# Kernel tuning notes

Hardware: AMD Instinct MI355X
Metric: run time of the kernel (lower is better)

Reference implementation:

```python
import jax, jax.numpy as jnp
import numpy as np

NUM_HEADS = 16


def setup_inputs() -> dict:
    key = jax.random.key(0)
    ks = jax.random.split(key, 6)
    B, S, D = 2, 2048, 1024
    hidden_states = jax.random.normal(ks[0], (B, S, D), dtype=jnp.float32)
    attention_mask = jnp.zeros((B, 1, 1, S), dtype=jnp.float32)  # additive mask
    # Linear weights stored as [in, out] (equivalent to torch weight.T)
    W_qkv = jax.random.normal(ks[1], (D, 3 * D), dtype=jnp.float32) * (1.0 / np.sqrt(D))
    b_qkv = jnp.zeros((3 * D,), dtype=jnp.float32)
    W_proj = jax.random.normal(ks[2], (D, D), dtype=jnp.float32) * (1.0 / np.sqrt(D))
    b_proj = jnp.zeros((D,), dtype=jnp.float32)
    return {
        "hidden_states": hidden_states,
        "attention_mask": attention_mask,
        "W_qkv": W_qkv,
        "b_qkv": b_qkv,
        "W_proj": W_proj,
        "b_proj": b_proj,
    }


def reference(hidden_states, attention_mask, W_qkv, b_qkv, W_proj, b_proj):
    B, S, D = hidden_states.shape
    H = NUM_HEADS
    hd = D // H
    scale = 1.0 / jnp.sqrt(jnp.asarray(hd, hidden_states.dtype))

    qkv = hidden_states @ W_qkv + b_qkv            # [B,S,3D]
    q, k, v = jnp.split(qkv, 3, axis=-1)
    # [B,S,D] -> [B,H,S,hd]
    split_heads = lambda t: t.reshape(B, S, H, hd).transpose(0, 2, 1, 3)
    q, k, v = split_heads(q), split_heads(k), split_heads(v)

    scores = jnp.einsum("bhqd,bhkd->bhqk", q, k) * scale + attention_mask
    attn = jax.nn.softmax(scores, axis=-1)
    ctx = jnp.einsum("bhqk,bhkd->bhqd", attn, v)   # [B,H,S,hd]
    ctx = ctx.transpose(0, 2, 1, 3).reshape(B, S, D)
    return ctx @ W_proj + b_proj
```

## Files before the change

kernel.cpp:

```cpp
#include <hip/hip_runtime.h>
#include <hip/hip_bf16.h>

typedef short short8 __attribute__((ext_vector_type(8)));
typedef float floatx4 __attribute__((ext_vector_type(4)));
typedef int intx4 __attribute__((ext_vector_type(4)));
typedef int intx2 __attribute__((ext_vector_type(2)));

#define S_LEN 2048
#define DMODEL 1024
#define NH 16
#define HD 64
#define BATCH 2

static __device__ __forceinline__ short f2bf(float x) {
    __hip_bfloat16 h = __float2bfloat16(x);
    return *(short*)&h;
}

static __device__ __forceinline__ unsigned pk2(float lo, float hi) {
    unsigned a = (unsigned)(unsigned short)f2bf(lo);
    unsigned b = (unsigned)(unsigned short)f2bf(hi);
    return a | (b << 16);
}

static __device__ __forceinline__ void async_ld16(const __hip_bfloat16* g, __hip_bfloat16* l) {
    __builtin_amdgcn_global_load_lds(
        (const __attribute__((address_space(1))) unsigned int*)g,
        (__attribute__((address_space(3))) unsigned int*)l, 16, 0, 0);
}

__global__ __launch_bounds__(256) void cvt_kernel(const float* __restrict__ X,
                                                  __hip_bfloat16* __restrict__ Y) {
    int i = (blockIdx.x * 256 + threadIdx.x) * 8;
    floatx4 f0 = *(const floatx4*)&X[i];
    floatx4 f1 = *(const floatx4*)&X[i + 4];
    short8 s;
    s[0] = f2bf(f0[0]); s[1] = f2bf(f0[1]); s[2] = f2bf(f0[2]); s[3] = f2bf(f0[3]);
    s[4] = f2bf(f1[0]); s[5] = f2bf(f1[1]); s[6] = f2bf(f1[2]); s[7] = f2bf(f1[3]);
    *(short8*)&Y[i] = s;
}

__global__ void transpose_kernel(const float* __restrict__ W,
                                 __hip_bfloat16* __restrict__ Wt, int K, int N) {
    __shared__ float tile[32][33];
    int n0 = blockIdx.x * 32, k0 = blockIdx.y * 32;
    int tx = threadIdx.x, ty = threadIdx.y;
#pragma unroll
    for (int i = 0; i < 32; i += 8)
        tile[ty + i][tx] = W[(size_t)(k0 + ty + i) * N + n0 + tx];
    __syncthreads();
#pragma unroll
    for (int i = 0; i < 32; i += 8)
        Wt[(size_t)(n0 + ty + i) * K + k0 + tx] = __float2bfloat16(tile[tx][ty + i]);
}

__global__ __launch_bounds__(256) void gemm128(
    const __hip_bfloat16* __restrict__ A, const __hip_bfloat16* __restrict__ Bt,
    const float* __restrict__ bias, float* __restrict__ Cf,
    __hip_bfloat16* __restrict__ Qp, __hip_bfloat16* __restrict__ Kp,
    __hip_bfloat16* __restrict__ Vt, int M, int N, int K, int mode) {
    __shared__ __align__(16) __hip_bfloat16 As[2][128 * 32];
    __shared__ __align__(16) __hip_bfloat16 Bs[2][128 * 32];
    const int gx = gridDim.x, gy = gridDim.y;
    const int flat = blockIdx.y * gx + blockIdx.x;
    const int cpx = (gx * gy) >> 3;
    const int id2 = (flat & 7) * cpx + (flat >> 3);
    const int m0 = (id2 % gy) * 128, n0 = (id2 / gy) * 128;
    const int t = threadIdx.x;
    const int wave = t >> 6, lane = t & 63;
    const int quad = lane >> 4, m16 = lane & 15;
    const int wm = (wave >> 1) * 64, wn = (wave & 1) * 64;
    const int srow = lane >> 2, scol = (lane & 3) * 8;

    const int rb0 = wave * 32, rb1 = wave * 32 + 16;
    const size_t aoff0 = (size_t)(m0 + rb0 + srow) * K + scol;
    const size_t aoff1 = (size_t)(m0 + rb1 + srow) * K + scol;
    const size_t boff0 = (size_t)(n0 + rb0 + srow) * K + scol;
    const size_t boff1 = (size_t)(n0 + rb1 + srow) * K + scol;

    async_ld16(&A[aoff0], &As[0][rb0 * 32]);
    async_ld16(&A[aoff1], &As[0][rb1 * 32]);
    async_ld16(&Bt[boff0], &Bs[0][rb0 * 32]);
    async_ld16(&Bt[boff1], &Bs[0][rb1 * 32]);
    __syncthreads();

    floatx4 acc[4][4] = {};
    const int NI = K >> 5;
    for (int it = 0; it < NI; ++it) {
        const int cur = it & 1;
        if (it < NI - 1) {
            const int k0 = (it + 1) * 32;
            async_ld16(&A[aoff0 + k0], &As[cur ^ 1][rb0 * 32]);
            async_ld16(&A[aoff1 + k0], &As[cur ^ 1][rb1 * 32]);
            async_ld16(&Bt[boff0 + k0], &Bs[cur ^ 1][rb0 * 32]);
            async_ld16(&Bt[boff1 + k0], &Bs[cur ^ 1][rb1 * 32]);
        }
        short8 af[4], bfr[4];
#pragma unroll
        for (int i = 0; i < 4; i++)
            af[i] = *(const short8*)&As[cur][(wm + i * 16 + m16) * 32 + quad * 8];
#pragma unroll
        for (int j = 0; j < 4; j++)
            bfr[j] = *(const short8*)&Bs[cur][(wn + j * 16 + m16) * 32 + quad * 8];
#pragma unroll
        for (int i = 0; i < 4; i++)
#pragma unroll
            for (int j = 0; j < 4; j++)
                acc[i][j] = __builtin_amdgcn_mfma_f32_16x16x32_bf16(af[i], bfr[j], acc[i][j], 0, 0, 0);
        __syncthreads();
    }
    if (mode == 0) {
#pragma unroll
        for (int i = 0; i < 4; i++)
#pragma unroll
            for (int j = 0; j < 4; j++) {
                int col = n0 + wn + j * 16 + m16;
                float bv = bias[col];
#pragma unroll
                for (int r = 0; r < 4; r++) {
                    int row = m0 + wm + i * 16 + quad * 4 + r;
                    Cf[(size_t)row * N + col] = acc[i][j][r] + bv;
                }
            }
    } else if (n0 < 2 * DMODEL) {
#pragma unroll
        for (int i = 0; i < 4; i++)
#pragma unroll
            for (int j = 0; j < 4; j++) {
                int col = n0 + wn + j * 16 + m16;
                float bv = bias[col];
#pragma unroll
                for (int r = 0; r < 4; r++) {
                    int row = m0 + wm + i * 16 + quad * 4 + r;
                    __hip_bfloat16 hv = __float2bfloat16(acc[i][j][r] + bv);
                    int tt = col >> 10, rem = col & 1023;
                    int h = rem >> 6, d = rem & 63;
                    int b = row >> 11, s = row & 2047;
                    if (tt == 0) Qp[((size_t)(b * NH + h) * S_LEN + s) * HD + d] = hv;
                    else         Kp[((size_t)(b * NH + h) * S_LEN + s) * HD + d] = hv;
                }
            }
    } else {
        char* T = (char*)As;
        const int bq = m0 >> 11;
        const int s_base = m0 & 2047;
        for (int p = 0; p < 4; p++) {
            if (wave == p) {
#pragma unroll
                for (int j = 0; j < 4; j++) {
                    const int drow = j * 16 + m16;
                    const float bv = bias[n0 + wn + j * 16 + m16];
                    const int within = (quad & 1) * 4;
#pragma unroll
                    for (int i = 0; i < 4; i++) {
                        const int colc = i * 2 + (quad >> 1);
                        const int physc = colc ^ (drow & 7);
                        intx2 v;
                        v[0] = (int)pk2(acc[i][j][0] + bv, acc[i][j][1] + bv);
                        v[1] = (int)pk2(acc[i][j][2] + bv, acc[i][j][3] + bv);
                        *(intx2*)(T + drow * 128 + physc * 16 + within * 2) = v;
                    }
                }
            }
            __syncthreads();
            {
                const int dl = t >> 2;
                const int sseg = (t & 3) * 16;
                const int c0 = (sseg >> 3) ^ (dl & 7);
                const int c1 = ((sseg >> 3) + 1) ^ (dl & 7);
                short8 a0 = *(const short8*)(T + dl * 128 + c0 * 16);
                short8 a1 = *(const short8*)(T + dl * 128 + c1 * 16);
                const int hh = (n0 - 2 * DMODEL + (p & 1) * 64) >> 6;
                const int sg = s_base + (p >> 1) * 64 + sseg;
                __hip_bfloat16* dst = &Vt[((size_t)(bq * NH + hh) * HD + dl) * S_LEN + sg];
                *(short8*)dst = a0;
                *(short8*)(dst + 8) = a1;
            }
            __syncthreads();
        }
    }
}

__global__ __launch_bounds__(512, 8) void attn_kernel(
    const __hip_bfloat16* __restrict__ Q,
    const __hip_bfloat16* __restrict__ K,
    const __hip_bfloat16* __restrict__ Vt,
    const float* __restrict__ mask,
    __hip_bfloat16* __restrict__ ctx) {
    __shared__ __align__(16) __hip_bfloat16 smem[16384];
    __shared__ float wsm[S_LEN];
    const int bh = blockIdx.x;
    const int b = bh >> 4, h = bh & 15;
    const int t = threadIdx.x, wave = t >> 6, lane = t & 63;
    const int team = wave >> 2, tw = wave & 3;
    const int quad = lane >> 4, m16 = lane & 15;
    const int qbase = blockIdx.y * 64 + tw * 16;
    const int ko = team * (S_LEN / 2);
    const __hip_bfloat16* Qh = Q + (size_t)bh * S_LEN * HD;
    const __hip_bfloat16* Kh = K + (size_t)bh * S_LEN * HD;
    const __hip_bfloat16* Vh = Vt + (size_t)bh * HD * S_LEN;
    const float* mb = mask + (size_t)b * S_LEN;
    const float LOG2E = 1.44269504f;
    const float scale2 = 0.125f * LOG2E;
    const float M_FIX2 = 20.0f * LOG2E;

    __hip_bfloat16* Ksb = smem + team * 8192;
    __hip_bfloat16* Vsb = smem + team * 8192 + 4096;

    {
        floatx4 mv = *(const floatx4*)&mb[t * 4];
        floatx4 wv;
#pragma unroll
        for (int r = 0; r < 4; r++) wv[r] = __builtin_fmaf(mv[r], LOG2E, -M_FIX2);
        *(floatx4*)&wsm[t * 4] = wv;
    }

    const int kr = lane >> 3, kc = lane & 7;
    const int kgoff = (tw * 8 + kr) * HD + ((kc ^ kr) * 8);
    const int vr = lane >> 2, vc = lane & 3;
    const int vd = tw * 16 + vr;
    const int vgoff = vd * S_LEN + (((vc ^ ((vd >> 1) & 3))) * 8);
    __hip_bfloat16* kdst0 = Ksb + tw * 512;
    __hip_bfloat16* kdst1 = Ksb + 2048 + tw * 512;
    __hip_bfloat16* vdst0 = Vsb + tw * 512;
    __hip_bfloat16* vdst1 = Vsb + 2048 + tw * 512;

    short8 aq0 = *(const short8*)&Qh[(size_t)(qbase + m16) * HD + quad * 8];
    short8 aq1 = *(const short8*)&Qh[(size_t)(qbase + m16) * HD + 32 + quad * 8];

    const short ONEB = (short)0x3F80;
    const short8 ones = {ONEB, ONEB, ONEB, ONEB, ONEB, ONEB, ONEB, ONEB};

    async_ld16(&Kh[(size_t)ko * HD + kgoff], kdst0);
    async_ld16(&Vh[(size_t)ko + vgoff], vdst0);
    __syncthreads();

    floatx4 o[4] = {};
    floatx4 lacc = {};
    const int swk = m16 & 7;
    const int e = quad & 1;
    const int C = ((quad & 1) << 1) | (quad >> 1);
    const int vsl = (C ^ ((m16 >> 1) & 3)) * 8;

    const int NIT = (S_LEN / 2) / 32;
    for (int it = 0; it < NIT; it++) {
        const int k0 = it * 32;
        const int cur = it & 1;
        if (it < NIT - 1) {
            async_ld16(&Kh[(size_t)(ko + k0 + 32) * HD + kgoff], cur ? kdst0 : kdst1);
            async_ld16(&Vh[(size_t)(ko + k0 + 32) + vgoff], cur ? vdst0 : vdst1);
        }

        const __hip_bfloat16* Kc = Ksb + cur * 2048;
        floatx4 sc[2] = {};
        __builtin_amdgcn_s_setprio(1);
#pragma unroll
        for (int kt = 0; kt < 2; kt++) {
            const int row = kt * 16 + m16;
            short8 ak0 = *(const short8*)&Kc[row * 64 + ((quad ^ swk) * 8)];
            short8 ak1 = *(const short8*)&Kc[row * 64 + (((quad + 4) ^ swk) * 8)];
            sc[kt] = __builtin_amdgcn_mfma_f32_16x16x32_bf16(ak0, aq0, sc[kt], 0, 0, 0);
            sc[kt] = __builtin_amdgcn_mfma_f32_16x16x32_bf16(ak1, aq1, sc[kt], 0, 0, 0);
        }
        __builtin_amdgcn_s_setprio(0);

        unsigned dk[2][2];
#pragma unroll
        for (int kt = 0; kt < 2; kt++) {
            floatx4 wv = *(const floatx4*)&wsm[ko + k0 + kt * 16 + quad * 4];
            float p0 = __builtin_amdgcn_exp2f(__builtin_fmaf(sc[kt][0], scale2, wv[0]));
            float p1 = __builtin_amdgcn_exp2f(__builtin_fmaf(sc[kt][1], scale2, wv[1]));
            float p2 = __builtin_amdgcn_exp2f(__builtin_fmaf(sc[kt][2], scale2, wv[2]));
            float p3 = __builtin_amdgcn_exp2f(__builtin_fmaf(sc[kt][3], scale2, wv[3]));
            dk[kt][0] = pk2(p0, p1);
            dk[kt][1] = pk2(p2, p3);
        }

        unsigned s0 = e ? dk[0][0] : dk[1][0];
        unsigned s1 = e ? dk[0][1] : dk[1][1];
        unsigned r0 = (unsigned)__builtin_amdgcn_ds_swizzle((int)s0, 0x401F);
        unsigned r1 = (unsigned)__builtin_amdgcn_ds_swizzle((int)s1, 0x401F);
        intx4 wa;
        wa[0] = (int)(e ? r0 : dk[0][0]);
        wa[1] = (int)(e ? r1 : dk[0][1]);
        wa[2] = (int)(e ? dk[1][0] : r0);
        wa[3] = (int)(e ? dk[1][1] : r1);
        short8 ap = *(short8*)&wa;

        const __hip_bfloat16* Vc = Vsb + cur * 2048;
        __builtin_amdgcn_s_setprio(1);
        lacc = __builtin_amdgcn_mfma_f32_16x16x32_bf16(ap, ones, lacc, 0, 0, 0);
#pragma unroll
        for (int tt = 0; tt < 4; tt++) {
            const int d = tt * 16 + m16;
            short8 bv = *(const short8*)&Vc[d * 32 + vsl];
            o[tt] = __builtin_amdgcn_mfma_f32_16x16x32_bf16(ap, bv, o[tt], 0, 0, 0);
        }
        __builtin_amdgcn_s_setprio(0);
        __syncthreads();
    }

    float* xch = (float*)smem;
    const int xi = (tw * 64 + lane) * 21;
    if (team == 1) {
#pragma unroll
        for (int tt = 0; tt < 4; tt++)
#pragma unroll
            for (int r = 0; r < 4; r++) xch[xi + tt * 4 + r] = o[tt][r];
#pragma unroll
        for (int r = 0; r < 4; r++) xch[xi + 16 + r] = lacc[r];
    }
    __syncthreads();
    if (team == 0) {
        float li[4];
#pragma unroll
        for (int r = 0; r < 4; r++) li[r] = 1.0f / (lacc[r] + xch[xi + 16 + r]);
#pragma unroll
        for (int tt = 0; tt < 4; tt++)
#pragma unroll
            for (int r = 0; r < 4; r++) {
                int srow = qbase + quad * 4 + r;
                int d = tt * 16 + m16;
                float v = (o[tt][r] + xch[xi + tt * 4 + r]) * li[r];
                ctx[((size_t)b * S_LEN + srow) * DMODEL + h * HD + d] = __float2bfloat16(v);
            }
    }
}

extern "C" void kernel_launch(void* const* d_in, const int* in_sizes, int n_in,
                              void* d_out, int out_size, void* d_ws, size_t ws_size,
                              hipStream_t stream) {
    (void)in_sizes; (void)n_in; (void)out_size; (void)ws_size;
    const float* hidden = (const float*)d_in[0];
    const float* mask   = (const float*)d_in[1];
    const float* Wqkv   = (const float*)d_in[2];
    const float* bqkv   = (const float*)d_in[3];
    const float* Wproj  = (const float*)d_in[4];
    const float* bproj  = (const float*)d_in[5];
    float* out = (float*)d_out;

    __hip_bfloat16* ws = (__hip_bfloat16*)d_ws;
    const size_t Q4 = 4u * 1024 * 1024;
    __hip_bfloat16* Qp      = ws;
    __hip_bfloat16* Kp      = ws + 1 * Q4;
    __hip_bfloat16* Vt      = ws + 2 * Q4;
    __hip_bfloat16* hid_bf  = ws + 3 * Q4;
    __hip_bfloat16* ctx     = ws + 3 * Q4;
    __hip_bfloat16* Wqkv_t  = ws + 4 * Q4;
    __hip_bfloat16* Wproj_t = ws + 4 * Q4;

    cvt_kernel<<<dim3(4 * 1024 * 1024 / 2048), 256, 0, stream>>>(hidden, hid_bf);
    transpose_kernel<<<dim3(3072 / 32, 1024 / 32), dim3(32, 8), 0, stream>>>(Wqkv, Wqkv_t, 1024, 3072);

    gemm128<<<dim3(3072 / 128, 4096 / 128), 256, 0, stream>>>(
        hid_bf, Wqkv_t, bqkv, nullptr, Qp, Kp, Vt, BATCH * S_LEN, 3 * DMODEL, DMODEL, 1);

    transpose_kernel<<<dim3(1024 / 32, 1024 / 32), dim3(32, 8), 0, stream>>>(Wproj, Wproj_t, 1024, 1024);

    attn_kernel<<<dim3(BATCH * NH, S_LEN / 64), 512, 0, stream>>>(Qp, Kp, Vt, mask, ctx);

    gemm128<<<dim3(1024 / 128, 4096 / 128), 256, 0, stream>>>(
        ctx, Wproj_t, bproj, out, nullptr, nullptr, nullptr, BATCH * S_LEN, DMODEL, DMODEL, 0);
}
```

Measured before the change: 215.2 us.

## Halve attention block to 4 waves, each computing two 16-row query tiles

The attention kernel now runs 256 threads (two teams of two waves) instead of 512, and each wave processes 32 query rows as two 16-row groups. Each K and V fragment read from shared memory is reused for two MFMA groups, and each thread issues twice as many async loads per tile. This cuts LDS reads per MFMA and the per-block wave count. The cost is more accumulator registers per wave and fewer waves to hide latency.

```diff
diff --git a/kernel.cpp b/kernel.cpp
--- a/kernel.cpp
+++ b/kernel.cpp
@@ -181,7 +181,7 @@
     }
 }
 
-__global__ __launch_bounds__(512, 8) void attn_kernel(
+__global__ __launch_bounds__(256, 4) void attn_kernel(
     const __hip_bfloat16* __restrict__ Q,
     const __hip_bfloat16* __restrict__ K,
     const __hip_bfloat16* __restrict__ Vt,
@@ -192,9 +192,9 @@
     const int bh = blockIdx.x;
     const int b = bh >> 4, h = bh & 15;
     const int t = threadIdx.x, wave = t >> 6, lane = t & 63;
-    const int team = wave >> 2, tw = wave & 3;
+    const int team = wave >> 1, tw = wave & 1;
     const int quad = lane >> 4, m16 = lane & 15;
-    const int qbase = blockIdx.y * 64 + tw * 16;
+    const int qbase = blockIdx.y * 64 + tw * 32;
     const int ko = team * (S_LEN / 2);
     const __hip_bfloat16* Qh = Q + (size_t)bh * S_LEN * HD;
     const __hip_bfloat16* Kh = K + (size_t)bh * S_LEN * HD;
@@ -207,36 +207,43 @@
     __hip_bfloat16* Ksb = smem + team * 8192;
     __hip_bfloat16* Vsb = smem + team * 8192 + 4096;
 
-    {
-        floatx4 mv = *(const floatx4*)&mb[t * 4];
+#pragma unroll
+    for (int i = 0; i < 2; i++) {
+        const int idx = (t + i * 256) * 4;
+        floatx4 mv = *(const floatx4*)&mb[idx];
         floatx4 wv;
 #pragma unroll
         for (int r = 0; r < 4; r++) wv[r] = __builtin_fmaf(mv[r], LOG2E, -M_FIX2);
-        *(floatx4*)&wsm[t * 4] = wv;
+        *(floatx4*)&wsm[idx] = wv;
     }
 
     const int kr = lane >> 3, kc = lane & 7;
-    const int kgoff = (tw * 8 + kr) * HD + ((kc ^ kr) * 8);
+    const int kgA = (tw * 16 + kr) * HD + ((kc ^ kr) * 8);
+    const int kgB = (tw * 16 + 8 + kr) * HD + ((kc ^ kr) * 8);
     const int vr = lane >> 2, vc = lane & 3;
-    const int vd = tw * 16 + vr;
-    const int vgoff = vd * S_LEN + (((vc ^ ((vd >> 1) & 3))) * 8);
-    __hip_bfloat16* kdst0 = Ksb + tw * 512;
-    __hip_bfloat16* kdst1 = Ksb + 2048 + tw * 512;
-    __hip_bfloat16* vdst0 = Vsb + tw * 512;
-    __hip_bfloat16* vdst1 = Vsb + 2048 + tw * 512;
-
-    short8 aq0 = *(const short8*)&Qh[(size_t)(qbase + m16) * HD + quad * 8];
-    short8 aq1 = *(const short8*)&Qh[(size_t)(qbase + m16) * HD + 32 + quad * 8];
+    const int vsw = (vc ^ ((vr >> 1) & 3)) * 8;
+    const int vgA = (tw * 32 + vr) * S_LEN + vsw;
+    const int vgB = (tw * 32 + 16 + vr) * S_LEN + vsw;
+    const int kd = tw * 1024, vd = tw * 1024;
+
+    short8 aq[2][2];
+#pragma unroll
+    for (int g = 0; g < 2; g++) {
+        aq[g][0] = *(const short8*)&Qh[(size_t)(qbase + g * 16 + m16) * HD + quad * 8];
+        aq[g][1] = *(const short8*)&Qh[(size_t)(qbase + g * 16 + m16) * HD + 32 + quad * 8];
+    }
 
     const short ONEB = (short)0x3F80;
     const short8 ones = {ONEB, ONEB, ONEB, ONEB, ONEB, ONEB, ONEB, ONEB};
 
-    async_ld16(&Kh[(size_t)ko * HD + kgoff], kdst0);
-    async_ld16(&Vh[(size_t)ko + vgoff], vdst0);
+    async_ld16(&Kh[(size_t)ko * HD + kgA], Ksb + kd);
+    async_ld16(&Kh[(size_t)ko * HD + kgB], Ksb + kd + 512);
+    async_ld16(&Vh[(size_t)ko + vgA], Vsb + vd);
+    async_ld16(&Vh[(size_t)ko + vgB], Vsb + vd + 512);
     __syncthreads();
 
-    floatx4 o[4] = {};
-    floatx4 lacc = {};
+    floatx4 o[2][4] = {};
+    floatx4 lacc[2] = {};
     const int swk = m16 & 7;
     const int e = quad & 1;
     const int C = ((quad & 1) << 1) | (quad >> 1);
@@ -247,83 +254,105 @@
         const int k0 = it * 32;
         const int cur = it & 1;
         if (it < NIT - 1) {
-            async_ld16(&Kh[(size_t)(ko + k0 + 32) * HD + kgoff], cur ? kdst0 : kdst1);
-            async_ld16(&Vh[(size_t)(ko + k0 + 32) + vgoff], cur ? vdst0 : vdst1);
+            const int nb = (cur ^ 1) * 2048;
+            async_ld16(&Kh[(size_t)(ko + k0 + 32) * HD + kgA], Ksb + nb + kd);
+            async_ld16(&Kh[(size_t)(ko + k0 + 32) * HD + kgB], Ksb + nb + kd + 512);
+            async_ld16(&Vh[(size_t)(ko + k0 + 32) + vgA], Vsb + nb + vd);
+            async_ld16(&Vh[(size_t)(ko + k0 + 32) + vgB], Vsb + nb + vd + 512);
         }
 
         const __hip_bfloat16* Kc = Ksb + cur * 2048;
-        floatx4 sc[2] = {};
+        floatx4 sc[2][2] = {};
         __builtin_amdgcn_s_setprio(1);
 #pragma unroll
         for (int kt = 0; kt < 2; kt++) {
             const int row = kt * 16 + m16;
             short8 ak0 = *(const short8*)&Kc[row * 64 + ((quad ^ swk) * 8)];
             short8 ak1 = *(const short8*)&Kc[row * 64 + (((quad + 4) ^ swk) * 8)];
-            sc[kt] = __builtin_amdgcn_mfma_f32_16x16x32_bf16(ak0, aq0, sc[kt], 0, 0, 0);
-            sc[kt] = __builtin_amdgcn_mfma_f32_16x16x32_bf16(ak1, aq1, sc[kt], 0, 0, 0);
+#pragma unroll
+            for (int g = 0; g < 2; g++) {
+                sc[g][kt] = __builtin_amdgcn_mfma_f32_16x16x32_bf16(ak0, aq[g][0], sc[g][kt], 0, 0, 0);
+                sc[g][kt] = __builtin_amdgcn_mfma_f32_16x16x32_bf16(ak1, aq[g][1], sc[g][kt], 0, 0, 0);
+            }
         }
         __builtin_amdgcn_s_setprio(0);
 
-        unsigned dk[2][2];
+        unsigned dk[2][2][2];
 #pragma unroll
         for (int kt = 0; kt < 2; kt++) {
             floatx4 wv = *(const floatx4*)&wsm[ko + k0 + kt * 16 + quad * 4];
-            float p0 = __builtin_amdgcn_exp2f(__builtin_fmaf(sc[kt][0], scale2, wv[0]));
-            float p1 = __builtin_amdgcn_exp2f(__builtin_fmaf(sc[kt][1], scale2, wv[1]));
-            float p2 = __builtin_amdgcn_exp2f(__builtin_fmaf(sc[kt][2], scale2, wv[2]));
-            float p3 = __builtin_amdgcn_exp2f(__builtin_fmaf(sc[kt][3], scale2, wv[3]));
-            dk[kt][0] = pk2(p0, p1);
-            dk[kt][1] = pk2(p2, p3);
-        }
-
-        unsigned s0 = e ? dk[0][0] : dk[1][0];
-        unsigned s1 = e ? dk[0][1] : dk[1][1];
-        unsigned r0 = (unsigned)__builtin_amdgcn_ds_swizzle((int)s0, 0x401F);
-        unsigned r1 = (unsigned)__builtin_amdgcn_ds_swizzle((int)s1, 0x401F);
-        intx4 wa;
-        wa[0] = (int)(e ? r0 : dk[0][0]);
-        wa[1] = (int)(e ? r1 : dk[0][1]);
-        wa[2] = (int)(e ? dk[1][0] : r0);
-        wa[3] = (int)(e ? dk[1][1] : r1);
-        short8 ap = *(short8*)&wa;
+#pragma unroll
+            for (int g = 0; g < 2; g++) {
+                float p0 = __builtin_amdgcn_exp2f(__builtin_fmaf(sc[g][kt][0], scale2, wv[0]));
+                float p1 = __builtin_amdgcn_exp2f(__builtin_fmaf(sc[g][kt][1], scale2, wv[1]));
+                float p2 = __builtin_amdgcn_exp2f(__builtin_fmaf(sc[g][kt][2], scale2, wv[2]));
+                float p3 = __builtin_amdgcn_exp2f(__builtin_fmaf(sc[g][kt][3], scale2, wv[3]));
+                dk[g][kt][0] = pk2(p0, p1);
+                dk[g][kt][1] = pk2(p2, p3);
+            }
+        }
+
+        short8 ap[2];
+#pragma unroll
+        for (int g = 0; g < 2; g++) {
+            unsigned s0 = e ? dk[g][0][0] : dk[g][1][0];
+            unsigned s1 = e ? dk[g][0][1] : dk[g][1][1];
+            unsigned r0 = (unsigned)__builtin_amdgcn_ds_swizzle((int)s0, 0x401F);
+            unsigned r1 = (unsigned)__builtin_amdgcn_ds_swizzle((int)s1, 0x401F);
+            intx4 wa;
+            wa[0] = (int)(e ? r0 : dk[g][0][0]);
+            wa[1] = (int)(e ? r1 : dk[g][0][1]);
+            wa[2] = (int)(e ? dk[g][1][0] : r0);
+            wa[3] = (int)(e ? dk[g][1][1] : r1);
+            ap[g] = *(short8*)&wa;
+        }
 
         const __hip_bfloat16* Vc = Vsb + cur * 2048;
         __builtin_amdgcn_s_setprio(1);
-        lacc = __builtin_amdgcn_mfma_f32_16x16x32_bf16(ap, ones, lacc, 0, 0, 0);
+        lacc[0] = __builtin_amdgcn_mfma_f32_16x16x32_bf16(ap[0], ones, lacc[0], 0, 0, 0);
+        lacc[1] = __builtin_amdgcn_mfma_f32_16x16x32_bf16(ap[1], ones, lacc[1], 0, 0, 0);
 #pragma unroll
         for (int tt = 0; tt < 4; tt++) {
             const int d = tt * 16 + m16;
             short8 bv = *(const short8*)&Vc[d * 32 + vsl];
-            o[tt] = __builtin_amdgcn_mfma_f32_16x16x32_bf16(ap, bv, o[tt], 0, 0, 0);
+            o[0][tt] = __builtin_amdgcn_mfma_f32_16x16x32_bf16(ap[0], bv, o[0][tt], 0, 0, 0);
+            o[1][tt] = __builtin_amdgcn_mfma_f32_16x16x32_bf16(ap[1], bv, o[1][tt], 0, 0, 0);
         }
         __builtin_amdgcn_s_setprio(0);
         __syncthreads();
     }
 
     float* xch = (float*)smem;
-    const int xi = (tw * 64 + lane) * 21;
     if (team == 1) {
 #pragma unroll
-        for (int tt = 0; tt < 4; tt++)
-#pragma unroll
-            for (int r = 0; r < 4; r++) xch[xi + tt * 4 + r] = o[tt][r];
-#pragma unroll
-        for (int r = 0; r < 4; r++) xch[xi + 16 + r] = lacc[r];
+        for (int g = 0; g < 2; g++) {
+            const int xi = ((tw * 2 + g) * 64 + lane) * 21;
+#pragma unroll
+            for (int tt = 0; tt < 4; tt++)
+#pragma unroll
+                for (int r = 0; r < 4; r++) xch[xi + tt * 4 + r] = o[g][tt][r];
+#pragma unroll
+            for (int r = 0; r < 4; r++) xch[xi + 16 + r] = lacc[g][r];
+        }
     }
     __syncthreads();
     if (team == 0) {
-        float li[4];
-#pragma unroll
-        for (int r = 0; r < 4; r++) li[r] = 1.0f / (lacc[r] + xch[xi + 16 + r]);
-#pragma unroll
-        for (int tt = 0; tt < 4; tt++)
-#pragma unroll
-            for (int r = 0; r < 4; r++) {
-                int srow = qbase + quad * 4 + r;
-                int d = tt * 16 + m16;
-                float v = (o[tt][r] + xch[xi + tt * 4 + r]) * li[r];
-                ctx[((size_t)b * S_LEN + srow) * DMODEL + h * HD + d] = __float2bfloat16(v);
-            }
+#pragma unroll
+        for (int g = 0; g < 2; g++) {
+            const int xi = ((tw * 2 + g) * 64 + lane) * 21;
+            float li[4];
+#pragma unroll
+            for (int r = 0; r < 4; r++) li[r] = 1.0f / (lacc[g][r] + xch[xi + 16 + r]);
+#pragma unroll
+            for (int tt = 0; tt < 4; tt++)
+#pragma unroll
+                for (int r = 0; r < 4; r++) {
+                    int srow = qbase + g * 16 + quad * 4 + r;
+                    int d = tt * 16 + m16;
+                    float v = (o[g][tt][r] + xch[xi + tt * 4 + r]) * li[r];
+                    ctx[((size_t)b * S_LEN + srow) * DMODEL + h * HD + d] = __float2bfloat16(v);
+                }
+        }
     }
 }
 
@@ -357,7 +386,7 @@
 
     transpose_kernel<<<dim3(1024 / 32, 1024 / 32), dim3(32, 8), 0, stream>>>(Wproj, Wproj_t, 1024, 1024);
 
-    attn_kernel<<<dim3(BATCH * NH, S_LEN / 64), 512, 0, stream>>>(Qp, Kp, Vt, mask, ctx);
+    attn_kernel<<<dim3(BATCH * NH, S_LEN / 64), 256, 0, stream>>>(Qp, Kp, Vt, mask, ctx);
 
     gemm128<<<dim3(1024 / 128, 4096 / 128), 256, 0, stream>>>(
         ctx, Wproj_t, bproj, out, nullptr, nullptr, nullptr, BATCH * S_LEN, DMODEL, DMODEL, 0);
```

After: 215.6 us. No clear change (+0.2%).
